# Performance work log

Hardware: AMD Instinct MI355X
Metric: run time of the kernel (lower is better)

Reference implementation:

```python
import jax, jax.numpy as jnp
import numpy as np

ALPHA = 0.2  # LeakyReLU negative slope


def gat_layer(x, W, a, alpha=ALPHA):
    """Multi-head dense GAT layer.
    x: (B, N, F); W: (H, F, O); a: (H, 2*O, 1).
    Returns (B, N, H*O) — ELU(head outputs) concatenated over heads.
    """
    H, F, O = W.shape
    Wh = jnp.einsum('bnf,hfo->bhno', x, W)          # (B,H,N,O)
    a_src = a[:, :O, 0]                              # (H,O)
    a_dst = a[:, O:, 0]                              # (H,O)
    s_src = jnp.einsum('bhno,ho->bhn', Wh, a_src)    # (B,H,N)
    s_dst = jnp.einsum('bhno,ho->bhn', Wh, a_dst)    # (B,H,N)
    e = s_src[..., :, None] + s_dst[..., None, :]    # (B,H,N,N)
    e = jax.nn.leaky_relu(e, negative_slope=alpha)
    att = jax.nn.softmax(e, axis=-1)                 # softmax over neighbors j
    out = jnp.einsum('bhnm,bhmo->bhno', att, Wh)     # (B,H,N,O)
    out = jax.nn.elu(out)
    B, _, N, _ = out.shape
    return jnp.transpose(out, (0, 2, 1, 3)).reshape(B, N, H * O)


def setup_inputs() -> dict:
    key = jax.random.key(0)
    ks = jax.random.split(key, 5)
    B, N = 32, 1024
    x = jax.random.normal(ks[0], (B, N, 4), dtype=jnp.float32)
    # layer1: nfeat=4, nhid=2, nheads=3
    W1 = jax.random.normal(ks[1], (3, 4, 2), dtype=jnp.float32) * 0.5
    a1 = jax.random.normal(ks[2], (3, 4, 1), dtype=jnp.float32) * 0.5
    # layer2: nfeat=6, nhid=4, nheads=1
    W2 = jax.random.normal(ks[3], (1, 6, 4), dtype=jnp.float32) * 0.5
    a2 = jax.random.normal(ks[4], (1, 8, 1), dtype=jnp.float32) * 0.5
    return {"x": x, "W1": W1, "a1": a1, "W2": W2, "a2": a2}


def reference(x, W1, a1, W2, a2):
    h = gat_layer(x, W1, a1)   # (B, N, 6)
    y = gat_layer(h, W2, a2)   # (B, N, 4)
    return y
```

## Files before the change

kernel.cpp:

```cpp
#include <hip/hip_runtime.h>


#define GAT_ALPHA 0.2f
#define LOG2E 1.44269504088896f

typedef float v2f __attribute__((ext_vector_type(2)));

template <int F, int O, int H, int RPB>
__global__ __launch_bounds__(256) void gat_layer_kernel(
    const float* __restrict__ x,
    const float* __restrict__ Wt,
    const float* __restrict__ at,
    float* __restrict__ out)
{
    constexpr int N = 1024, NT = 256, S = 16;
    constexpr int NP = N / 2;
    constexpr int R = RPB / 16;
    constexpr int Q = O + 1;
    constexpr int CHUNKS = N / RPB;
    constexpr int PAD = R * Q + 1;

    const int bid   = blockIdx.x;
    const int chunk = bid % CHUNKS;
    const int h     = (bid / CHUNKS) % H;
    const int b     = bid / (CHUNKS * H);
    const int tid   = threadIdx.x;
    const int wv    = tid >> 6, l = tid & 63;
    const int r     = (l >> 2) & 15;
    const int sq    = l & 3;
    const int s     = (wv << 2) | sq;

    float Wl[F][O];
#pragma unroll
    for (int f = 0; f < F; ++f)
#pragma unroll
        for (int o = 0; o < O; ++o) Wl[f][o] = Wt[(h * F + f) * O + o];
    float asrc[O], adst[O];
#pragma unroll
    for (int o = 0; o < O; ++o) {
        asrc[o] = at[h * 2 * O + o];
        adst[o] = at[h * 2 * O + O + o];
    }

    __shared__ float4 sE[NP];
    __shared__ float4 sW01[NP];
    __shared__ float4 sW23[(O > 2) ? NP : 1];
    __shared__ float  sredu[4 * 16 * PAD];

    const float* xb = x + (size_t)b * N * F;
#pragma unroll
    for (int qq = 0; qq < NP / NT; ++qq) {
        const int q = qq * NT + tid;
        float xv[2][F];
        if constexpr (F == 4) {
            const float4 va = ((const float4*)xb)[2 * q];
            const float4 vb = ((const float4*)xb)[2 * q + 1];
            xv[0][0] = va.x; xv[0][1] = va.y; xv[0][2] = va.z; xv[0][3] = va.w;
            xv[1][0] = vb.x; xv[1][1] = vb.y; xv[1][2] = vb.z; xv[1][3] = vb.w;
        } else {
            const float4* x4 = (const float4*)xb;
            const float2* x2 = (const float2*)xb;
            const float4 fa = x4[3 * q];
            const float2 fb = x2[6 * q + 2];
            const float2 fc = x2[6 * q + 3];
            const float4 fd = x4[3 * q + 2];
            xv[0][0] = fa.x; xv[0][1] = fa.y; xv[0][2] = fa.z; xv[0][3] = fa.w;
            xv[0][4] = fb.x; xv[0][5] = fb.y;
            xv[1][0] = fc.x; xv[1][1] = fc.y;
            xv[1][2] = fd.x; xv[1][3] = fd.y; xv[1][4] = fd.z; xv[1][5] = fd.w;
        }
        float wh[2][O], d[2];
#pragma unroll
        for (int p = 0; p < 2; ++p) {
            d[p] = 0.0f;
#pragma unroll
            for (int o = 0; o < O; ++o) {
                float acc = 0.0f;
#pragma unroll
                for (int f = 0; f < F; ++f) acc += xv[p][f] * Wl[f][o];
                wh[p][o] = acc; d[p] += acc * adst[o];
            }
        }
        const float t0 = d[0] * LOG2E, t1 = d[1] * LOG2E;
        sE[q] = make_float4(__builtin_amdgcn_exp2f(t0),
                            __builtin_amdgcn_exp2f(t1),
                            __builtin_amdgcn_exp2f(GAT_ALPHA * t0),
                            __builtin_amdgcn_exp2f(GAT_ALPHA * t1));
        sW01[q] = make_float4(wh[0][0], wh[1][0], wh[0][1], wh[1][1]);
        if constexpr (O > 2)
            sW23[q] = make_float4(wh[0][2], wh[1][2], wh[0][3], wh[1][3]);
    }
    __syncthreads();

    float rho[R];
#pragma unroll
    for (int j = 0; j < R; ++j) {
        const int row = chunk * RPB + r + 16 * j;
        const int qr = row >> 1, cp = row & 1;
        const float4 w01 = sW01[qr];
        float sn = (cp ? w01.y : w01.x) * asrc[0] + (cp ? w01.w : w01.z) * asrc[1];
        if constexpr (O > 2) {
            const float4 w23 = sW23[qr];
            sn += (cp ? w23.y : w23.x) * asrc[2] + (cp ? w23.w : w23.z) * asrc[3];
        }
        rho[j] = __builtin_amdgcn_exp2f(0.8f * LOG2E * sn);
    }

    v2f den[R], num[R][O];
#pragma unroll
    for (int j = 0; j < R; ++j) {
        den[j] = (v2f)(0.0f);
#pragma unroll
        for (int o = 0; o < O; ++o) num[j][o] = (v2f)(0.0f);
    }

#pragma unroll 4
    for (int p = 0; p < NP / S; ++p) {
        const int q = p * S + s;
        const float4 e4 = sE[q];
        const float4 w4 = sW01[q];
        const v2f E1 = {e4.x, e4.y}, E2 = {e4.z, e4.w};
        const v2f W0 = {w4.x, w4.y}, W1v = {w4.z, w4.w};
        v2f W2v, W3v;
        if constexpr (O > 2) {
            const float4 w4b = sW23[q];
            W2v = (v2f){w4b.x, w4b.y}; W3v = (v2f){w4b.z, w4b.w};
        }
#pragma unroll
        for (int j = 0; j < R; ++j) {
            const v2f t = rho[j] * E1;
            v2f w;
            w.x = fmaxf(t.x, E2.x);
            w.y = fmaxf(t.y, E2.y);
            den[j] += w;
            num[j][0] += w * W0;
            num[j][1] += w * W1v;
            if constexpr (O > 2) {
                num[j][2] += w * W2v;
                num[j][3] += w * W3v;
            }
        }
    }

#pragma unroll
    for (int j = 0; j < R; ++j) {
        float dn = den[j].x + den[j].y;
        dn += __shfl_xor(dn, 1, 64);
        dn += __shfl_xor(dn, 2, 64);
        float nm[O];
#pragma unroll
        for (int o = 0; o < O; ++o) {
            nm[o] = num[j][o].x + num[j][o].y;
            nm[o] += __shfl_xor(nm[o], 1, 64);
            nm[o] += __shfl_xor(nm[o], 2, 64);
        }
        if (sq == 0) {
            const int base = (wv * 16 + r) * PAD + j * Q;
            sredu[base] = dn;
#pragma unroll
            for (int o = 0; o < O; ++o) sredu[base + 1 + o] = nm[o];
        }
    }
    __syncthreads();

    for (int idx = tid; idx < RPB * O; idx += NT) {
        const int rowl = idx / O, o = idx % O;
        const int rr = rowl & 15, jj = rowl >> 4;
        float dn = 0.0f, nm = 0.0f;
#pragma unroll
        for (int ww = 0; ww < 4; ++ww) {
            const int base = (ww * 16 + rr) * PAD + jj * Q;
            dn += sredu[base];
            nm += sredu[base + 1 + o];
        }
        float v = nm / dn;
        v = (v > 0.0f) ? v : (__expf(v) - 1.0f);
        const int row = chunk * RPB + rowl;
        out[((size_t)b * N + row) * (H * O) + h * O + o] = v;
    }
}

extern "C" void kernel_launch(void* const* d_in, const int* in_sizes, int n_in,
                              void* d_out, int out_size, void* d_ws, size_t ws_size,
                              hipStream_t stream) {
    const float* x  = (const float*)d_in[0];
    const float* W1 = (const float*)d_in[1];
    const float* a1 = (const float*)d_in[2];
    const float* W2 = (const float*)d_in[3];
    const float* a2 = (const float*)d_in[4];

    float* h1 = (float*)d_ws;
    float* y  = (float*)d_out;

    constexpr int B = 32;
    gat_layer_kernel<4, 2, 3, 64><<<B * 3 * 16, 256, 0, stream>>>(x, W1, a1, h1);
    gat_layer_kernel<6, 4, 1, 32><<<B * 1 * 32, 256, 0, stream>>>(h1, W2, a2, y);
}
```

Measured before the change: 82.34 us.

## Replace dense N×N attention sweep with key-bucketed prefix/suffix sums

The dense O(N^2) softmax-weighted sum is replaced by a sort-like bucketing of destination scores into 512 buckets. Prefix sums of exp(alpha*d) terms and suffix sums of exp(d) terms are precomputed with LDS atomics and wave scans. Each row then handles all full buckets with two lookups and iterates only over its own boundary bucket. This cuts per-block work from all N pairs to roughly N plus a small bucket scan. In exchange it adds atomics, several syncs and redundant per-block bucketing of the full graph, and it can be load-imbalanced if keys cluster into one bucket.

```diff
diff --git a/kernel.cpp b/kernel.cpp
--- a/kernel.cpp
+++ b/kernel.cpp
@@ -4,179 +4,216 @@
 #define GAT_ALPHA 0.2f
 #define LOG2E 1.44269504088896f
 
-typedef float v2f __attribute__((ext_vector_type(2)));
+__device__ __forceinline__ float ex2(float v) { return __builtin_amdgcn_exp2f(v); }
 
 template <int F, int O, int H, int RPB>
-__global__ __launch_bounds__(256) void gat_layer_kernel(
+__global__ __launch_bounds__(256) void gat_bucket_kernel(
     const float* __restrict__ x,
     const float* __restrict__ Wt,
     const float* __restrict__ at,
     float* __restrict__ out)
 {
-    constexpr int N = 1024, NT = 256, S = 16;
-    constexpr int NP = N / 2;
-    constexpr int R = RPB / 16;
-    constexpr int Q = O + 1;
+    constexpr int N = 1024, NT = 256, EPT = N / NT;
+    constexpr int NB = 512;
     constexpr int CHUNKS = N / RPB;
-    constexpr int PAD = R * Q + 1;
+    constexpr int A1 = O + 1;
 
     const int bid   = blockIdx.x;
     const int chunk = bid % CHUNKS;
     const int h     = (bid / CHUNKS) % H;
     const int b     = bid / (CHUNKS * H);
     const int tid   = threadIdx.x;
-    const int wv    = tid >> 6, l = tid & 63;
-    const int r     = (l >> 2) & 15;
-    const int sq    = l & 3;
-    const int s     = (wv << 2) | sq;
-
-    float Wl[F][O];
+    const int wv    = tid >> 6, ln = tid & 63;
+
+    float Wl[F][O], asrc[O], adst[O];
 #pragma unroll
     for (int f = 0; f < F; ++f)
 #pragma unroll
         for (int o = 0; o < O; ++o) Wl[f][o] = Wt[(h * F + f) * O + o];
-    float asrc[O], adst[O];
 #pragma unroll
     for (int o = 0; o < O; ++o) {
         asrc[o] = at[h * 2 * O + o];
         adst[o] = at[h * 2 * O + O + o];
     }
 
-    __shared__ float4 sE[NP];
-    __shared__ float4 sW01[NP];
-    __shared__ float4 sW23[(O > 2) ? NP : 1];
-    __shared__ float  sredu[4 * 16 * PAD];
-
+    __shared__ float sSrc[N];
+    __shared__ int   sCS[NB + 1];
+    __shared__ float sKey[N];
+    __shared__ float sWhS[O][N];
+    __shared__ float sPre[A1][NB + 1];
+    __shared__ float sSuf[A1][NB + 1];
+    __shared__ float sMM[8];
+    __shared__ int   sRedI[4];
+    __shared__ float sRedF[2][A1][4];
+
+    for (int i = tid; i < NB + 1; i += NT) sCS[i] = 0;
+    for (int i = tid; i < A1 * (NB + 1); i += NT) {
+        (&sPre[0][0])[i] = 0.0f;
+        (&sSuf[0][0])[i] = 0.0f;
+    }
+
+    float key[EPT], wh[EPT][O];
+    float kmin = 3.4e38f, kmax = -3.4e38f;
     const float* xb = x + (size_t)b * N * F;
 #pragma unroll
-    for (int qq = 0; qq < NP / NT; ++qq) {
-        const int q = qq * NT + tid;
-        float xv[2][F];
+    for (int k = 0; k < EPT; ++k) {
+        const int m = k * NT + tid;
+        float xv[F];
         if constexpr (F == 4) {
-            const float4 va = ((const float4*)xb)[2 * q];
-            const float4 vb = ((const float4*)xb)[2 * q + 1];
-            xv[0][0] = va.x; xv[0][1] = va.y; xv[0][2] = va.z; xv[0][3] = va.w;
-            xv[1][0] = vb.x; xv[1][1] = vb.y; xv[1][2] = vb.z; xv[1][3] = vb.w;
+            const float4 v = ((const float4*)xb)[m];
+            xv[0] = v.x; xv[1] = v.y; xv[2] = v.z; xv[3] = v.w;
         } else {
-            const float4* x4 = (const float4*)xb;
             const float2* x2 = (const float2*)xb;
-            const float4 fa = x4[3 * q];
-            const float2 fb = x2[6 * q + 2];
-            const float2 fc = x2[6 * q + 3];
-            const float4 fd = x4[3 * q + 2];
-            xv[0][0] = fa.x; xv[0][1] = fa.y; xv[0][2] = fa.z; xv[0][3] = fa.w;
-            xv[0][4] = fb.x; xv[0][5] = fb.y;
-            xv[1][0] = fc.x; xv[1][1] = fc.y;
-            xv[1][2] = fd.x; xv[1][3] = fd.y; xv[1][4] = fd.z; xv[1][5] = fd.w;
-        }
-        float wh[2][O], d[2];
-#pragma unroll
-        for (int p = 0; p < 2; ++p) {
-            d[p] = 0.0f;
-#pragma unroll
-            for (int o = 0; o < O; ++o) {
-                float acc = 0.0f;
-#pragma unroll
-                for (int f = 0; f < F; ++f) acc += xv[p][f] * Wl[f][o];
-                wh[p][o] = acc; d[p] += acc * adst[o];
-            }
-        }
-        const float t0 = d[0] * LOG2E, t1 = d[1] * LOG2E;
-        sE[q] = make_float4(__builtin_amdgcn_exp2f(t0),
-                            __builtin_amdgcn_exp2f(t1),
-                            __builtin_amdgcn_exp2f(GAT_ALPHA * t0),
-                            __builtin_amdgcn_exp2f(GAT_ALPHA * t1));
-        sW01[q] = make_float4(wh[0][0], wh[1][0], wh[0][1], wh[1][1]);
-        if constexpr (O > 2)
-            sW23[q] = make_float4(wh[0][2], wh[1][2], wh[0][3], wh[1][3]);
-    }
-    __syncthreads();
-
-    float rho[R];
-#pragma unroll
-    for (int j = 0; j < R; ++j) {
-        const int row = chunk * RPB + r + 16 * j;
-        const int qr = row >> 1, cp = row & 1;
-        const float4 w01 = sW01[qr];
-        float sn = (cp ? w01.y : w01.x) * asrc[0] + (cp ? w01.w : w01.z) * asrc[1];
-        if constexpr (O > 2) {
-            const float4 w23 = sW23[qr];
-            sn += (cp ? w23.y : w23.x) * asrc[2] + (cp ? w23.w : w23.z) * asrc[3];
-        }
-        rho[j] = __builtin_amdgcn_exp2f(0.8f * LOG2E * sn);
-    }
-
-    v2f den[R], num[R][O];
-#pragma unroll
-    for (int j = 0; j < R; ++j) {
-        den[j] = (v2f)(0.0f);
-#pragma unroll
-        for (int o = 0; o < O; ++o) num[j][o] = (v2f)(0.0f);
-    }
-
-#pragma unroll 4
-    for (int p = 0; p < NP / S; ++p) {
-        const int q = p * S + s;
-        const float4 e4 = sE[q];
-        const float4 w4 = sW01[q];
-        const v2f E1 = {e4.x, e4.y}, E2 = {e4.z, e4.w};
-        const v2f W0 = {w4.x, w4.y}, W1v = {w4.z, w4.w};
-        v2f W2v, W3v;
-        if constexpr (O > 2) {
-            const float4 w4b = sW23[q];
-            W2v = (v2f){w4b.x, w4b.y}; W3v = (v2f){w4b.z, w4b.w};
-        }
-#pragma unroll
-        for (int j = 0; j < R; ++j) {
-            const v2f t = rho[j] * E1;
-            v2f w;
-            w.x = fmaxf(t.x, E2.x);
-            w.y = fmaxf(t.y, E2.y);
-            den[j] += w;
-            num[j][0] += w * W0;
-            num[j][1] += w * W1v;
-            if constexpr (O > 2) {
-                num[j][2] += w * W2v;
-                num[j][3] += w * W3v;
-            }
-        }
-    }
-
-#pragma unroll
-    for (int j = 0; j < R; ++j) {
-        float dn = den[j].x + den[j].y;
-        dn += __shfl_xor(dn, 1, 64);
-        dn += __shfl_xor(dn, 2, 64);
-        float nm[O];
+            const float2 va = x2[3 * m], vb = x2[3 * m + 1], vc = x2[3 * m + 2];
+            xv[0] = va.x; xv[1] = va.y; xv[2] = vb.x;
+            xv[3] = vb.y; xv[4] = vc.x; xv[5] = vc.y;
+        }
+        float d = 0.0f, sn = 0.0f;
 #pragma unroll
         for (int o = 0; o < O; ++o) {
-            nm[o] = num[j][o].x + num[j][o].y;
-            nm[o] += __shfl_xor(nm[o], 1, 64);
-            nm[o] += __shfl_xor(nm[o], 2, 64);
-        }
-        if (sq == 0) {
-            const int base = (wv * 16 + r) * PAD + j * Q;
-            sredu[base] = dn;
-#pragma unroll
-            for (int o = 0; o < O; ++o) sredu[base + 1 + o] = nm[o];
-        }
-    }
-    __syncthreads();
-
-    for (int idx = tid; idx < RPB * O; idx += NT) {
-        const int rowl = idx / O, o = idx % O;
-        const int rr = rowl & 15, jj = rowl >> 4;
-        float dn = 0.0f, nm = 0.0f;
-#pragma unroll
-        for (int ww = 0; ww < 4; ++ww) {
-            const int base = (ww * 16 + rr) * PAD + jj * Q;
-            dn += sredu[base];
-            nm += sredu[base + 1 + o];
-        }
-        float v = nm / dn;
-        v = (v > 0.0f) ? v : (__expf(v) - 1.0f);
-        const int row = chunk * RPB + rowl;
-        out[((size_t)b * N + row) * (H * O) + h * O + o] = v;
+            float acc = 0.0f;
+#pragma unroll
+            for (int f = 0; f < F; ++f) acc += xv[f] * Wl[f][o];
+            wh[k][o] = acc;
+            d += acc * adst[o];
+            sn += acc * asrc[o];
+        }
+        key[k] = d;
+        sSrc[m] = sn;
+        kmin = fminf(kmin, d);
+        kmax = fmaxf(kmax, d);
+    }
+#pragma unroll
+    for (int s = 1; s < 64; s <<= 1) {
+        kmin = fminf(kmin, __shfl_xor(kmin, s, 64));
+        kmax = fmaxf(kmax, __shfl_xor(kmax, s, 64));
+    }
+    if (ln == 0) { sMM[wv] = kmin; sMM[4 + wv] = kmax; }
+    __syncthreads();
+
+    kmin = fminf(fminf(sMM[0], sMM[1]), fminf(sMM[2], sMM[3]));
+    kmax = fmaxf(fmaxf(sMM[4], sMM[5]), fmaxf(sMM[6], sMM[7]));
+    const float invw = (float)NB / fmaxf(kmax - kmin, 1e-30f);
+
+    int bk[EPT], rk[EPT];
+#pragma unroll
+    for (int k = 0; k < EPT; ++k) {
+        int q = (int)((key[k] - kmin) * invw);
+        q = q < 0 ? 0 : (q > NB - 1 ? NB - 1 : q);
+        bk[k] = q;
+        rk[k] = atomicAdd(&sCS[q], 1);
+        const float e1 = ex2(LOG2E * key[k]);
+        const float e2 = ex2(GAT_ALPHA * LOG2E * key[k]);
+        atomicAdd(&sSuf[0][q], e1);
+        atomicAdd(&sPre[0][q], e2);
+#pragma unroll
+        for (int o = 0; o < O; ++o) {
+            atomicAdd(&sSuf[1 + o][q], e1 * wh[k][o]);
+            atomicAdd(&sPre[1 + o][q], e2 * wh[k][o]);
+        }
+    }
+    __syncthreads();
+
+    const int c0 = sCS[2 * tid], c1 = sCS[2 * tid + 1];
+    float p0[A1], p1[A1], s0[A1], s1[A1];
+#pragma unroll
+    for (int a = 0; a < A1; ++a) {
+        p0[a] = sPre[a][2 * tid]; p1[a] = sPre[a][2 * tid + 1];
+        s0[a] = sSuf[a][2 * tid]; s1[a] = sSuf[a][2 * tid + 1];
+    }
+    int irun = c0 + c1;
+#pragma unroll
+    for (int s = 1; s < 64; s <<= 1) {
+        const int u = __shfl_up(irun, s, 64);
+        if (ln >= s) irun += u;
+    }
+    if (ln == 63) sRedI[wv] = irun;
+    int irex = __shfl_up(irun, 1, 64);
+    if (ln == 0) irex = 0;
+
+    float prun[A1], prex[A1], srun[A1], srex[A1];
+#pragma unroll
+    for (int a = 0; a < A1; ++a) {
+        prun[a] = p0[a] + p1[a];
+#pragma unroll
+        for (int s = 1; s < 64; s <<= 1) {
+            const float u = __shfl_up(prun[a], s, 64);
+            if (ln >= s) prun[a] += u;
+        }
+        if (ln == 63) sRedF[0][a][wv] = prun[a];
+        prex[a] = __shfl_up(prun[a], 1, 64);
+        if (ln == 0) prex[a] = 0.0f;
+
+        srun[a] = s0[a] + s1[a];
+#pragma unroll
+        for (int s = 1; s < 64; s <<= 1) {
+            const float u = __shfl_down(srun[a], s, 64);
+            if (ln < 64 - s) srun[a] += u;
+        }
+        if (ln == 0) sRedF[1][a][wv] = srun[a];
+        srex[a] = __shfl_down(srun[a], 1, 64);
+        if (ln == 63) srex[a] = 0.0f;
+    }
+    __syncthreads();
+
+    {
+        int ibase = 0;
+        for (int w = 0; w < 4; ++w) if (w < wv) ibase += sRedI[w];
+        const int iex = ibase + irex;
+        sCS[2 * tid] = iex;
+        sCS[2 * tid + 1] = iex + c0;
+        if (tid == 0) sCS[NB] = N;
+    }
+#pragma unroll
+    for (int a = 0; a < A1; ++a) {
+        float pbase = 0.0f, sbase = 0.0f;
+        for (int w = 0; w < 4; ++w) {
+            if (w < wv) pbase += sRedF[0][a][w];
+            if (w > wv) sbase += sRedF[1][a][w];
+        }
+        const float pex = pbase + prex[a];
+        sPre[a][2 * tid] = pex;
+        sPre[a][2 * tid + 1] = pex + p0[a];
+        const float sex = sbase + srex[a];
+        sSuf[a][2 * tid + 1] = sex + s1[a];
+        sSuf[a][2 * tid] = sex + s1[a] + s0[a];
+    }
+    __syncthreads();
+
+#pragma unroll
+    for (int k = 0; k < EPT; ++k) {
+        const int pos = sCS[bk[k]] + rk[k];
+        sKey[pos] = key[k];
+#pragma unroll
+        for (int o = 0; o < O; ++o) sWhS[o][pos] = wh[k][o];
+    }
+    __syncthreads();
+
+    for (int rr = tid; rr < RPB; rr += NT) {
+        const int row = chunk * RPB + rr;
+        const float sn = sSrc[row];
+        const float rho = ex2(0.8f * LOG2E * sn);
+        int bq = (int)((-sn - kmin) * invw);
+        bq = bq < 0 ? 0 : (bq > NB - 1 ? NB - 1 : bq);
+        const int i0 = sCS[bq], i1 = sCS[bq + 1];
+        float den = rho * sSuf[0][bq + 1] + sPre[0][bq];
+        float num[O];
+#pragma unroll
+        for (int o = 0; o < O; ++o)
+            num[o] = rho * sSuf[1 + o][bq + 1] + sPre[1 + o][bq];
+        for (int i = i0; i < i1; ++i) {
+            const float kk = sKey[i];
+            const float w = fmaxf(rho * ex2(LOG2E * kk), ex2(GAT_ALPHA * LOG2E * kk));
+            den += w;
+#pragma unroll
+            for (int o = 0; o < O; ++o) num[o] += w * sWhS[o][i];
+        }
+#pragma unroll
+        for (int o = 0; o < O; ++o) {
+            float v = num[o] / den;
+            v = (v > 0.0f) ? v : (__expf(v) - 1.0f);
+            out[((size_t)b * N + row) * (H * O) + h * O + o] = v;
+        }
     }
 }
 
@@ -193,6 +230,6 @@
     float* y  = (float*)d_out;
 
     constexpr int B = 32;
-    gat_layer_kernel<4, 2, 3, 64><<<B * 3 * 16, 256, 0, stream>>>(x, W1, a1, h1);
-    gat_layer_kernel<6, 4, 1, 32><<<B * 1 * 32, 256, 0, stream>>>(h1, W2, a2, y);
+    gat_bucket_kernel<4, 2, 3, 128><<<B * 3 * (1024 / 128), 256, 0, stream>>>(x, W1, a1, h1);
+    gat_bucket_kernel<6, 4, 1, 64><<<B * 1 * (1024 / 64), 256, 0, stream>>>(h1, W2, a2, y);
 }
```

Measured after the change: 124.0 us. 1.51x slower.
